# Kernel optimization log

Hardware: AMD Instinct MI355X
Metric: run time of the kernel (lower is better)

## Reference

```python
import jax, jax.numpy as jnp
import numpy as np

N, D, C, R, O = 256, 64, 32, 16, 32  # batch, features, in-channels (left=right), repetitions, out-channels


def setup_inputs() -> dict:
    key = jax.random.key(0)
    k1, k2, k3 = jax.random.split(key, 3)
    left_ll = jax.random.normal(k1, (N, D, C, R), dtype=jnp.float32)
    right_ll = jax.random.normal(k2, (N, D, C, R), dtype=jnp.float32)
    logits = jax.random.normal(k3, (D, O, R, C, C), dtype=jnp.float32)
    return {"left_ll": left_ll, "right_ll": right_ll, "logits": logits}


def reference(left_ll, right_ll, logits):
    # Normalized weights: softmax over flattened (i, j) channel-pair axis.
    f, co, r, i, j = logits.shape
    weights = jax.nn.softmax(logits.reshape(f, co, r, i * j), axis=-1).reshape(f, co, r, i, j)

    # LogEinsumExp trick: subtract per-(feature, rep) channel max, exponentiate,
    # contract in linear space, then return to log space.
    left_max = jnp.max(left_ll, axis=2, keepdims=True)    # (N, D, 1, R)
    right_max = jnp.max(right_ll, axis=2, keepdims=True)  # (N, D, 1, R)
    left_prob = jnp.exp(left_ll - left_max)
    right_prob = jnp.exp(right_ll - right_max)

    # (N, D, O, R) weighted cross-product over left/right channels.
    prob = jnp.einsum('ndir,ndjr,dorij->ndor', left_prob, right_prob, weights)
    return jnp.log(prob) + left_max + right_max  # maxes broadcast over out-channel axis
```

## Files before the change

kernel.cpp:

```cpp
#include <hip/hip_runtime.h>

#define N_ 256
#define D_ 64
#define C_ 32
#define R_ 16
#define O_ 32

typedef _Float16 half8 __attribute__((ext_vector_type(8)));
typedef float f32x16 __attribute__((ext_vector_type(16)));

__global__ __launch_bounds__(256) void prep_kernel(
    const float* __restrict__ left, const float* __restrict__ right,
    _Float16* __restrict__ lw, _Float16* __restrict__ rw,
    float* __restrict__ msum) {
  const int b = blockIdx.x, t = threadIdx.x;
  const int n = ((b >> 3) << 1) | (t >> 7);
  const int d = ((b & 7) << 3) | ((t >> 4) & 7);
  const int r = t & 15;
  const size_t sbase = ((size_t)(n * D_ + d) * C_) * R_ + r;
  const size_t dbase = (size_t)((d * R_ + r) * N_ + n) * C_;

  float lmx = -1e30f, rmx = -1e30f;
  {
    float vals[C_];
#pragma unroll
    for (int i = 0; i < C_; i++) {
      float v = left[sbase + (size_t)i * R_];
      vals[i] = v;
      lmx = fmaxf(lmx, v);
    }
    half8 pk[4];
#pragma unroll
    for (int i = 0; i < C_; i++) pk[i >> 3][i & 7] = (_Float16)__expf(vals[i] - lmx);
    half8* dst = (half8*)(lw + dbase);
#pragma unroll
    for (int q = 0; q < 4; q++) dst[q] = pk[q];
  }
  {
    float vals[C_];
#pragma unroll
    for (int i = 0; i < C_; i++) {
      float v = right[sbase + (size_t)i * R_];
      vals[i] = v;
      rmx = fmaxf(rmx, v);
    }
    half8 pk[4];
#pragma unroll
    for (int i = 0; i < C_; i++) pk[i >> 3][i & 7] = (_Float16)__expf(vals[i] - rmx);
    half8* dst = (half8*)(rw + dbase);
#pragma unroll
    for (int q = 0; q < 4; q++) dst[q] = pk[q];
  }
  msum[(d * R_ + r) * N_ + n] = lmx + rmx;
}

__global__ __launch_bounds__(256, 2) void main_kernel(
    const float* __restrict__ logits, const _Float16* __restrict__ lw,
    const _Float16* __restrict__ rw, const float* __restrict__ msum,
    float* __restrict__ out) {
  __shared__ _Float16 Wl[64 * 64 * 8];
  __shared__ float psum[4][64];
  __shared__ float msum_s[N_];

  const int bid = blockIdx.x;
  const int workid = ((bid & 7) << 7) | (bid >> 3);
  const int d = workid >> 4, r = workid & 15;

  const int t = threadIdx.x;
  const int w = t >> 6, l = t & 63;
  const int o = l & 31, jb = l >> 5;

  msum_s[t] = msum[(d * R_ + r) * N_ + t];

  const float* lg = logits + ((size_t)((d * O_ + o) * R_ + r) * C_) * C_;
  float lsum = 0.f;
#pragma unroll
  for (int ii = 0; ii < 4; ii++) {
    const int i = (jb << 4) | (w << 2) | ii;
    float vv[C_];
    const float4* rp = (const float4*)(lg + i * C_);
#pragma unroll
    for (int q = 0; q < 8; q++) {
      float4 f = rp[q];
      vv[q * 4 + 0] = f.x;
      vv[q * 4 + 1] = f.y;
      vv[q * 4 + 2] = f.z;
      vv[q * 4 + 3] = f.w;
    }
#pragma unroll
    for (int q2 = 0; q2 < 4; q2++) {
      const int s = (w << 4) | (ii << 2) | q2;
      half8 hh;
#pragma unroll
      for (int p = 0; p < 8; p++) {
        float e = __expf(vv[(q2 << 3) | p]);
        lsum += e;
        hh[p] = (_Float16)e;
      }
      *(half8*)&Wl[((s << 6) | l) << 3] = hh;
    }
  }
  psum[w][l] = lsum;
  __syncthreads();
  float tot = 0.f;
#pragma unroll
  for (int ww = 0; ww < 4; ww++) tot += psum[ww][o] + psum[ww][o + 32];
  const float rlogsum = __logf(tot);

  const _Float16* lbase = lw + (size_t)((d * R_ + r) * N_) * C_;
  const _Float16* rbase = rw + (size_t)((d * R_ + r) * N_) * C_;
  half8 Lh[2][2], Rh[2][4];
#pragma unroll
  for (int mb = 0; mb < 2; mb++) {
    const int row = (w << 6) | (mb << 5) | o;
    const half8* lp = (const half8*)(lbase + row * C_ + (jb << 4));
    Lh[mb][0] = lp[0];
    Lh[mb][1] = lp[1];
    const half8* rp2 = (const half8*)(rbase + row * C_);
#pragma unroll
    for (int q = 0; q < 4; q++) Rh[mb][q] = rp2[q];
  }

  f32x16 acc[2];
#pragma unroll
  for (int mb = 0; mb < 2; mb++)
#pragma unroll
    for (int g = 0; g < 16; g++) acc[mb][g] = 0.f;

#pragma unroll
  for (int s = 0; s < 64; s++) {
    const half8 Bf = *(const half8*)&Wl[((s << 6) | l) << 3];
    const int ig = s >> 2, qq = s & 3;
#pragma unroll
    for (int mb = 0; mb < 2; mb++) {
      const _Float16 Lsc = Lh[mb][ig >> 3][ig & 7];
      const half8 Ld = {Lsc, Lsc, Lsc, Lsc, Lsc, Lsc, Lsc, Lsc};
      const half8 Af = Ld * Rh[mb][qq];
      acc[mb] = __builtin_amdgcn_mfma_f32_32x32x16_f16(Af, Bf, acc[mb], 0, 0, 0);
    }
  }

#pragma unroll
  for (int mb = 0; mb < 2; mb++) {
#pragma unroll
    for (int g = 0; g < 16; g++) {
      const int rowt = (g & 3) + ((g >> 2) << 3) + (jb << 2);
      const int n = (w << 6) | (mb << 5) | rowt;
      const float val = __logf(acc[mb][g]) - rlogsum + msum_s[n];
      out[(((size_t)n * D_ + d) * O_ + o) * R_ + r] = val;
    }
  }
}

extern "C" void kernel_launch(void* const* d_in, const int* in_sizes, int n_in,
                              void* d_out, int out_size, void* d_ws, size_t ws_size,
                              hipStream_t stream) {
  const float* left = (const float*)d_in[0];
  const float* right = (const float*)d_in[1];
  const float* logits = (const float*)d_in[2];
  float* out = (float*)d_out;
  _Float16* lw = (_Float16*)d_ws;
  _Float16* rw = (_Float16*)((char*)d_ws + (size_t)16 * 1024 * 1024);
  float* ms = (float*)((char*)d_ws + (size_t)32 * 1024 * 1024);

  prep_kernel<<<1024, 256, 0, stream>>>(left, right, lw, rw, ms);
  main_kernel<<<1024, 256, 0, stream>>>(logits, lw, rw, ms, out);
}
```

Measured before the change: 303.7 us.

## Split weight staging into two halves and overlap logits load with MFMA

Main kernel grows to 512 threads, each wave owning one 32-row batch tile, and stages the softmax weights in two 32-slot halves through a smaller shared buffer. The second half of logits is loaded from global memory while the first half's MFMAs run. L/R operand loads are hoisted before the weight exponentiation. The aim is to halve LDS use, raise occupancy and hide logits load latency, at the cost of extra barriers and fewer MFMAs per wave.

```diff
diff --git a/kernel.cpp b/kernel.cpp
--- a/kernel.cpp
+++ b/kernel.cpp
@@ -54,12 +54,12 @@
   msum[(d * R_ + r) * N_ + n] = lmx + rmx;
 }
 
-__global__ __launch_bounds__(256, 2) void main_kernel(
+__global__ __launch_bounds__(512, 4) void main_kernel(
     const float* __restrict__ logits, const _Float16* __restrict__ lw,
     const _Float16* __restrict__ rw, const float* __restrict__ msum,
     float* __restrict__ out) {
-  __shared__ _Float16 Wl[64 * 64 * 8];
-  __shared__ float psum[4][64];
+  __shared__ _Float16 Wl[32 * 64 * 8];
+  __shared__ float psum[16][32];
   __shared__ float msum_s[N_];
 
   const int bid = blockIdx.x;
@@ -70,85 +70,105 @@
   const int w = t >> 6, l = t & 63;
   const int o = l & 31, jb = l >> 5;
 
-  msum_s[t] = msum[(d * R_ + r) * N_ + t];
+  const _Float16* lbase = lw + (size_t)((d * R_ + r) * N_) * C_;
+  const _Float16* rbase = rw + (size_t)((d * R_ + r) * N_) * C_;
+  const int row = (w << 5) | o;
+  const half8* lp = (const half8*)(lbase + row * C_ + (jb << 4));
+  const half8 LhA = lp[0];
+  const half8 LhB = lp[1];
+  const half8* rp2 = (const half8*)(rbase + row * C_);
+  half8 Rh[4];
+#pragma unroll
+  for (int q = 0; q < 4; q++) Rh[q] = rp2[q];
 
-  const float* lg = logits + ((size_t)((d * O_ + o) * R_ + r) * C_) * C_;
+  if (t < N_) msum_s[t] = msum[(d * R_ + r) * N_ + t];
+
+  const int o_a = t & 31, ih = t >> 5;
+  const float* lgrow =
+      logits + ((size_t)((d * O_ + o_a) * R_ + r) * C_) * C_;
+  const int i0 = ((ih >> 3) << 4) | (ih & 7);
+  const int slot = ((ih >> 3) << 5) | o_a;
+  const int sbase_a = (ih & 7) << 2;
+
   float lsum = 0.f;
+
+  float4 v0[8];
+  {
+    const float4* rp = (const float4*)(lgrow + i0 * C_);
 #pragma unroll
-  for (int ii = 0; ii < 4; ii++) {
-    const int i = (jb << 4) | (w << 2) | ii;
-    float vv[C_];
-    const float4* rp = (const float4*)(lg + i * C_);
+    for (int q = 0; q < 8; q++) v0[q] = rp[q];
+  }
 #pragma unroll
-    for (int q = 0; q < 8; q++) {
-      float4 f = rp[q];
-      vv[q * 4 + 0] = f.x;
-      vv[q * 4 + 1] = f.y;
-      vv[q * 4 + 2] = f.z;
-      vv[q * 4 + 3] = f.w;
+  for (int q2 = 0; q2 < 4; q2++) {
+    half8 hh;
+    float tmp[8] = {v0[q2 * 2].x,     v0[q2 * 2].y,     v0[q2 * 2].z,
+                    v0[q2 * 2].w,     v0[q2 * 2 + 1].x, v0[q2 * 2 + 1].y,
+                    v0[q2 * 2 + 1].z, v0[q2 * 2 + 1].w};
+#pragma unroll
+    for (int p = 0; p < 8; p++) {
+      float e = __expf(tmp[p]);
+      lsum += e;
+      hh[p] = (_Float16)e;
     }
+    *(half8*)&Wl[(((sbase_a | q2) << 6) | slot) << 3] = hh;
+  }
+  __syncthreads();
+
+  float4 v1[8];
+  {
+    const float4* rp = (const float4*)(lgrow + (i0 + 8) * C_);
 #pragma unroll
-    for (int q2 = 0; q2 < 4; q2++) {
-      const int s = (w << 4) | (ii << 2) | q2;
-      half8 hh;
+    for (int q = 0; q < 8; q++) v1[q] = rp[q];
+  }
+
+  f32x16 acc;
 #pragma unroll
-      for (int p = 0; p < 8; p++) {
-        float e = __expf(vv[(q2 << 3) | p]);
-        lsum += e;
-        hh[p] = (_Float16)e;
-      }
-      *(half8*)&Wl[((s << 6) | l) << 3] = hh;
+  for (int g = 0; g < 16; g++) acc[g] = 0.f;
+
+#pragma unroll
+  for (int s = 0; s < 32; s++) {
+    const half8 Bf = *(const half8*)&Wl[((s << 6) | l) << 3];
+    const _Float16 Lsc = LhA[s >> 2];
+    const half8 Ld = {Lsc, Lsc, Lsc, Lsc, Lsc, Lsc, Lsc, Lsc};
+    acc = __builtin_amdgcn_mfma_f32_32x32x16_f16(Ld * Rh[s & 3], Bf, acc, 0, 0, 0);
+  }
+  __syncthreads();
+
+#pragma unroll
+  for (int q2 = 0; q2 < 4; q2++) {
+    half8 hh;
+    float tmp[8] = {v1[q2 * 2].x,     v1[q2 * 2].y,     v1[q2 * 2].z,
+                    v1[q2 * 2].w,     v1[q2 * 2 + 1].x, v1[q2 * 2 + 1].y,
+                    v1[q2 * 2 + 1].z, v1[q2 * 2 + 1].w};
+#pragma unroll
+    for (int p = 0; p < 8; p++) {
+      float e = __expf(tmp[p]);
+      lsum += e;
+      hh[p] = (_Float16)e;
     }
+    *(half8*)&Wl[(((sbase_a | q2) << 6) | slot) << 3] = hh;
   }
-  psum[w][l] = lsum;
+  psum[ih][o_a] = lsum;
   __syncthreads();
+
+#pragma unroll
+  for (int s = 0; s < 32; s++) {
+    const half8 Bf = *(const half8*)&Wl[((s << 6) | l) << 3];
+    const _Float16 Lsc = LhB[s >> 2];
+    const half8 Ld = {Lsc, Lsc, Lsc, Lsc, Lsc, Lsc, Lsc, Lsc};
+    acc = __builtin_amdgcn_mfma_f32_32x32x16_f16(Ld * Rh[s & 3], Bf, acc, 0, 0, 0);
+  }
+
   float tot = 0.f;
 #pragma unroll
-  for (int ww = 0; ww < 4; ww++) tot += psum[ww][o] + psum[ww][o + 32];
+  for (int k = 0; k < 16; k++) tot += psum[k][o];
   const float rlogsum = __logf(tot);
 
-  const _Float16* lbase = lw + (size_t)((d * R_ + r) * N_) * C_;
-  const _Float16* rbase = rw + (size_t)((d * R_ + r) * N_) * C_;
-  half8 Lh[2][2], Rh[2][4];
 #pragma unroll
-  for (int mb = 0; mb < 2; mb++) {
-    const int row = (w << 6) | (mb << 5) | o;
-    const half8* lp = (const half8*)(lbase + row * C_ + (jb << 4));
-    Lh[mb][0] = lp[0];
-    Lh[mb][1] = lp[1];
-    const half8* rp2 = (const half8*)(rbase + row * C_);
-#pragma unroll
-    for (int q = 0; q < 4; q++) Rh[mb][q] = rp2[q];
-  }
-
-  f32x16 acc[2];
-#pragma unroll
-  for (int mb = 0; mb < 2; mb++)
-#pragma unroll
-    for (int g = 0; g < 16; g++) acc[mb][g] = 0.f;
-
-#pragma unroll
-  for (int s = 0; s < 64; s++) {
-    const half8 Bf = *(const half8*)&Wl[((s << 6) | l) << 3];
-    const int ig = s >> 2, qq = s & 3;
-#pragma unroll
-    for (int mb = 0; mb < 2; mb++) {
-      const _Float16 Lsc = Lh[mb][ig >> 3][ig & 7];
-      const half8 Ld = {Lsc, Lsc, Lsc, Lsc, Lsc, Lsc, Lsc, Lsc};
-      const half8 Af = Ld * Rh[mb][qq];
-      acc[mb] = __builtin_amdgcn_mfma_f32_32x32x16_f16(Af, Bf, acc[mb], 0, 0, 0);
-    }
-  }
-
-#pragma unroll
-  for (int mb = 0; mb < 2; mb++) {
-#pragma unroll
-    for (int g = 0; g < 16; g++) {
-      const int rowt = (g & 3) + ((g >> 2) << 3) + (jb << 2);
-      const int n = (w << 6) | (mb << 5) | rowt;
-      const float val = __logf(acc[mb][g]) - rlogsum + msum_s[n];
-      out[(((size_t)n * D_ + d) * O_ + o) * R_ + r] = val;
-    }
+  for (int g = 0; g < 16; g++) {
+    const int n = (w << 5) | ((g & 3) + ((g >> 2) << 3) + (jb << 2));
+    const float val = __logf(acc[g]) - rlogsum + msum_s[n];
+    out[(((size_t)n * D_ + d) * O_ + o) * R_ + r] = val;
   }
 }
 
@@ -164,5 +184,5 @@
   float* ms = (float*)((char*)d_ws + (size_t)32 * 1024 * 1024);
 
   prep_kernel<<<1024, 256, 0, stream>>>(left, right, lw, rw, ms);
-  main_kernel<<<1024, 256, 0, stream>>>(logits, lw, rw, ms, out);
+  main_kernel<<<1024, 512, 0, stream>>>(logits, lw, rw, ms, out);
 }
```

After: 303.0 us. No clear change (-0.2%).
